# Kernel tuning notes

Hardware: AMD Instinct MI355X
Metric: run time of the kernel (lower is better)

The kernel has to match this reference:

```python
import jax, jax.numpy as jnp
from jax import lax
import numpy as np

B, H, W = 2048, 28, 28
LATENT_EACH = 64
LATENT = 2 * LATENT_EACH  # 128
MEM_SIZE = 8192
TOPK = 10
EPS = 1e-12


def _conv(x, w, b):
    # x: NCHW, w: OIHW, 3x3 conv, padding=1 (SAME)
    y = lax.conv_general_dilated(x, w, (1, 1), 'SAME',
                                 dimension_numbers=('NCHW', 'OIHW', 'NCHW'))
    return y + b[None, :, None, None]


def _deconv(x, w, b):
    # ConvTranspose2d(k=4, stride=2, padding=1) -> out = 2*in (SAME transpose)
    # w: HWIO = (4,4,in,out)
    y = lax.conv_transpose(x, w, (2, 2), 'SAME',
                           dimension_numbers=('NCHW', 'HWIO', 'NCHW'))
    return y + b[None, :, None, None]


def _encoder(x, w1, b1, w2, b2, fcw, fcb):
    h = jax.nn.relu(_conv(x, w1, b1))
    h = jax.nn.relu(_conv(h, w2, b2))
    feat = h.mean(axis=(2, 3))  # AdaptiveAvgPool2d((1,1)) + flatten -> [B,64]
    return feat @ fcw.T + fcb


def _memory_match(z, mem):
    mn = mem / jnp.maximum(jnp.linalg.norm(mem, axis=1, keepdims=True), EPS)
    zn = z / jnp.maximum(jnp.linalg.norm(z, axis=1, keepdims=True), EPS)
    sim = zn @ mn.T                      # [B, MEM_SIZE]
    topv, topi = lax.top_k(sim, TOPK)    # [B, K]
    wts = jax.nn.softmax(topv, axis=1)   # [B, K]
    sel = mem[topi]                      # gather: [B, K, LATENT]
    return jnp.einsum('bk,bkd->bd', wts, sel)


def setup_inputs() -> dict:
    key = jax.random.key(0)
    ks = jax.random.split(key, 24)
    g = lambda k, s, scale=0.05: jax.random.normal(k, s, jnp.float32) * scale
    inp = {
        'x': jax.random.normal(ks[0], (B, 1, H, W), jnp.float32),
        # center encoder
        'ce_w1': g(ks[1], (32, 1, 3, 3)), 'ce_b1': jnp.zeros((32,), jnp.float32),
        'ce_w2': g(ks[2], (64, 32, 3, 3)), 'ce_b2': jnp.zeros((64,), jnp.float32),
        'ce_fcw': g(ks[3], (LATENT_EACH, 64)), 'ce_fcb': jnp.zeros((LATENT_EACH,), jnp.float32),
        # global encoder
        'ge_w1': g(ks[4], (32, 1, 3, 3)), 'ge_b1': jnp.zeros((32,), jnp.float32),
        'ge_w2': g(ks[5], (64, 32, 3, 3)), 'ge_b2': jnp.zeros((64,), jnp.float32),
        'ge_fcw': g(ks[6], (LATENT_EACH, 64)), 'ge_fcb': jnp.zeros((LATENT_EACH,), jnp.float32),
        # memory bank (Parameter ~ randn)
        'mem': jax.random.normal(ks[7], (MEM_SIZE, LATENT), jnp.float32),
        # decoder
        'dec_fcw': g(ks[8], (64 * 7 * 7, LATENT)), 'dec_fcb': jnp.zeros((64 * 7 * 7,), jnp.float32),
        'd_w1': g(ks[9], (4, 4, 64, 32)), 'd_b1': jnp.zeros((32,), jnp.float32),   # deconv 64->32
        'd_w2': g(ks[10], (16, 32, 3, 3)), 'd_b2': jnp.zeros((16,), jnp.float32),  # conv 32->16
        'd_w3': g(ks[11], (4, 4, 16, 8)), 'd_b3': jnp.zeros((8,), jnp.float32),    # deconv 16->8
        'd_w4': g(ks[12], (1, 8, 3, 3)), 'd_b4': jnp.zeros((1,), jnp.float32),     # conv 8->1
    }
    return inp


def reference(x, ce_w1, ce_b1, ce_w2, ce_b2, ce_fcw, ce_fcb,
              ge_w1, ge_b1, ge_w2, ge_b2, ge_fcw, ge_fcb,
              mem, dec_fcw, dec_fcb,
              d_w1, d_b1, d_w2, d_b2, d_w3, d_b3, d_w4, d_b4):
    # crop_center(x, 14): start = (28-14)//2 = 7
    x_center = x[:, :, 7:21, 7:21]
    z_center = _encoder(x_center, ce_w1, ce_b1, ce_w2, ce_b2, ce_fcw, ce_fcb)
    z_global = _encoder(x, ge_w1, ge_b1, ge_w2, ge_b2, ge_fcw, ge_fcb)
    z = jnp.concatenate([z_center, z_global], axis=1)  # [B, 128]
    z_match = _memory_match(z, mem)                    # [B, 128]
    d = (z_match @ dec_fcw.T + dec_fcb).reshape(B, 64, 7, 7)
    d = jax.nn.relu(_deconv(d, d_w1, d_b1))   # [B,32,14,14]
    d = jax.nn.relu(_conv(d, d_w2, d_b2))     # [B,16,14,14]
    d = jax.nn.relu(_deconv(d, d_w3, d_b3))   # [B,8,28,28]
    x_hat = _conv(d, d_w4, d_b4)              # [B,1,28,28]
    return x_hat
```

## Files before the change

kernel.cpp:

```cpp
#include <hip/hip_runtime.h>
#include <cfloat>
#include <cmath>

#define TPB 256

typedef _Float16 half8 __attribute__((ext_vector_type(8)));
typedef float floatx16 __attribute__((ext_vector_type(16)));
typedef float floatx4 __attribute__((ext_vector_type(4)));

__device__ __forceinline__ float wave_reduce_sum(float v) {
#pragma unroll
  for (int off = 32; off > 0; off >>= 1) v += __shfl_xor(v, off, 64);
  return v;
}

__global__ __launch_bounds__(64) void prep_bfrags(
    const float* __restrict__ ce_w2, const float* __restrict__ ge_w2,
    float* __restrict__ frags) {
  const int blk = blockIdx.x;
  const int enc = blk / 72;
  const int frag = blk % 72;
  const int ks = frag >> 2, part = (frag >> 1) & 1, nt = frag & 1;
  const int tap = ks >> 1, half = ks & 1;
  const int lane = threadIdx.x;
  const float* w2 = enc ? ge_w2 : ce_w2;
  const int n = nt * 32 + (lane & 31);
  const int cb = half * 16 + (lane >> 5) * 8;
  half8 out;
#pragma unroll
  for (int j = 0; j < 8; ++j) {
    float v = w2[(n * 32 + cb + j) * 9 + tap];
    _Float16 h = (_Float16)v;
    out[j] = (part == 0) ? h : (_Float16)((v - (float)h) * 4096.f);
  }
  *(half8*)((char*)frags + ((size_t)blk * 64 + lane) * 16) = out;
}

__global__ __launch_bounds__(64) void prep_dec1(
    const float* __restrict__ w1, float* __restrict__ frags) {
  const int blk = blockIdx.x;
  const int phase = blk >> 4, ks = blk & 15;
  const int pa = phase >> 1, pb = phase & 1;
  const int st = ks >> 2, kk = ks & 3;
  const int s = st >> 1, tt = st & 1;
  const int lane = threadIdx.x;
  const int kg = lane >> 5, n = lane & 31;
  const int tap = (pa + 2 * s) * 4 + (pb + 2 * tt);
  half8 o;
#pragma unroll
  for (int j = 0; j < 8; ++j) {
    int c = kk * 16 + kg * 8 + j;
    o[j] = (_Float16)w1[tap * 2048 + c * 32 + n];
  }
  *(half8*)((char*)frags + ((size_t)blk * 64 + lane) * 16) = o;
}

__global__ __launch_bounds__(64) void prep_dfc(
    const float* __restrict__ dfcw, float* __restrict__ frags) {
  const int blk = blockIdx.x;
  const int nt = blk >> 3, ks = blk & 7;
  const int lane = threadIdx.x;
  const int n = lane & 31, kg = lane >> 5;
  const int j = nt * 32 + n;
  const int px = j >> 6, c = j & 63;
  half8 o;
#pragma unroll
  for (int u = 0; u < 8; ++u)
    o[u] = (_Float16)dfcw[(size_t)(c * 49 + px) * 128 + ks * 16 + kg * 8 + u];
  *(half8*)((char*)frags + ((size_t)blk * 64 + lane) * 16) = o;
}

__global__ __launch_bounds__(64) void prep_mem(
    const float* __restrict__ memg, float* __restrict__ frags) {
  const int blk = blockIdx.x;
  const int slot = blk & 15;
  const int p = slot >> 3, ks = slot & 7;
  const int T = blk >> 4;
  const int lane = threadIdx.x;
  const int n = lane & 31, kg = lane >> 5;
  const float* src = memg + (size_t)(T * 32 + n) * 128 + ks * 16 + kg * 8;
  half8 o;
#pragma unroll
  for (int j = 0; j < 8; ++j) {
    float v = src[j];
    _Float16 h = (_Float16)v;
    o[j] = p ? (_Float16)((v - (float)h) * 4096.f) : h;
  }
  *(half8*)((char*)frags + ((size_t)blk * 64 + lane) * 16) = o;
}

__global__ __launch_bounds__(256) void norm_kernel(
    const float* __restrict__ memg, float* __restrict__ invn) {
  const int wv = threadIdx.x >> 6, lane = threadIdx.x & 63;
  const int row = blockIdx.x * 4 + wv;
  const float* r = memg + (size_t)row * 128;
  float a = r[lane], b = r[lane + 64];
  float s = wave_reduce_sum(a * a + b * b);
  if (lane == 0) invn[row] = 1.f / fmaxf(sqrtf(s), 1e-12f);
}

template <int S, bool CENTER>
__device__ __forceinline__ void encoder_body(
    char* smem, const float* __restrict__ x, const float* __restrict__ w1,
    const float* __restrict__ b1, const float* __restrict__ b2,
    const float* __restrict__ fcw, const float* __restrict__ fcb,
    const float* __restrict__ bfrag, float* __restrict__ zout, int zoff,
    int b) {
  constexpr int SP = S + 2;
  constexpr int NBANDS = (S == 28) ? 3 : 2;
  constexpr int RMAX = 12;
  constexpr int NPIX = RMAX * SP;
  constexpr int GSTB = NPIX * 16;
  constexpr int PSTB = 4 * GSTB;

  char* h1s = smem;
  float* xs = (float*)(smem + 2 * PSTB);
  float* w1s = xs + SP * SP;
  float* featp = w1s + 288;

  const int t = threadIdx.x;
  const int lane = t & 63;
  const int wv = t >> 6;
  const int ntW = wv & 1;

  for (int e = t; e < SP * SP; e += TPB) xs[e] = 0.f;
  for (int e = t; e < 288; e += TPB) w1s[e] = w1[e];
  __syncthreads();
  const float* xb = x + (size_t)b * 784 + (CENTER ? (7 * 28 + 7) : 0);
  for (int e = t; e < S * S; e += TPB) {
    int i = e / S, j = e - i * S;
    xs[(i + 1) * SP + (j + 1)] = xb[i * 28 + j];
  }

  float sp = 0.f;
  const float biasW = b2[ntW * 32 + (lane & 31)];
  const int gOff = (lane >> 5) * GSTB;
  const char* bgbase = (const char*)bfrag + lane * 16;

#pragma unroll
  for (int band = 0; band < NBANDS; ++band) {
    const int BH_ = (S == 28) ? ((band < 2) ? 10 : 8) : ((band == 0) ? 10 : 4);
    const int b0 = band * 10;
    const int LIMIT = BH_ * S;
    const int MTB = (LIMIT + 31) / 32;

    __syncthreads();
    for (int e = t; e < 4 * NPIX; e += TPB) {
      int g = e / NPIX;
      int pix = e - g * NPIX;
      int lr = pix / SP;
      int cw = pix - lr * SP;
      int gr = b0 - 1 + lr;
      int ebase = g * GSTB + pix * 16;
      half8 hi8 = {}, lo8 = {};
      if (gr >= 0 && gr < S && cw >= 1 && cw <= S) {
        float xv[9];
#pragma unroll
        for (int di = 0; di < 3; ++di)
#pragma unroll
          for (int dj = 0; dj < 3; ++dj)
            xv[di * 3 + dj] = xs[(gr + di) * SP + (cw - 1 + dj)];
#pragma unroll
        for (int u = 0; u < 8; ++u) {
          int ch = g * 8 + u;
          float a = b1[ch];
#pragma unroll
          for (int v = 0; v < 9; ++v) a += xv[v] * w1s[ch * 9 + v];
          a = fmaxf(a, 0.f);
          _Float16 h = (_Float16)a;
          hi8[u] = h;
          lo8[u] = (_Float16)((a - (float)h) * 4096.f);
        }
      }
      *(half8*)(h1s + ebase) = hi8;
      *(half8*)(h1s + PSTB + ebase) = lo8;
    }
    __syncthreads();
#pragma unroll 1
    for (int u = wv; u < 2 * MTB; u += 4) {
      const int mt = u >> 1;
      floatx16 accH = {}, accL = {};
      int px = mt * 32 + (lane & 31);
      px = px < LIMIT ? px : LIMIT - 1;
      const int r = px / S, cc = px - r * S;
      const int pixB = (r * SP + cc) * 16;
#pragma unroll 3
      for (int tap = 0; tap < 9; ++tap) {
        const int di = tap / 3, dj = tap - di * 3;
        const int offT = (di * SP + dj) * 16;
#pragma unroll
        for (int half = 0; half < 2; ++half) {
          const int ks = tap * 2 + half;
          const char* bp = bgbase + ks * 4096 + ntW * 1024;
          const int offA = pixB + offT + gOff + half * (2 * GSTB);
          half8 ah = *(const half8*)(h1s + offA);
          half8 al = *(const half8*)(h1s + PSTB + offA);
          half8 bh = *(const half8*)(bp);
          half8 bl = *(const half8*)(bp + 2048);
          accH = __builtin_amdgcn_mfma_f32_32x32x16_f16(ah, bh, accH, 0, 0, 0);
          accL = __builtin_amdgcn_mfma_f32_32x32x16_f16(ah, bl, accL, 0, 0, 0);
          accL = __builtin_amdgcn_mfma_f32_32x32x16_f16(al, bh, accL, 0, 0, 0);
        }
      }
#pragma unroll
      for (int reg = 0; reg < 16; ++reg) {
        int row = (reg & 3) + 8 * (reg >> 2) + 4 * (lane >> 5);
        int p = mt * 32 + row;
        if (p < LIMIT)
          sp += fmaxf(accH[reg] + accL[reg] * (1.f / 4096.f) + biasW, 0.f);
      }
    }
  }
  sp += __shfl_xor(sp, 32);
  if (lane < 32) featp[wv * 32 + lane] = sp;
  __syncthreads();
  if (t < 64) featp[t] = (featp[t] + featp[64 + t]) * (1.f / (S * S));
  __syncthreads();
  if (t < 64) {
    float s = 0.f;
#pragma unroll
    for (int i = 0; i < 64; ++i) s += featp[i] * fcw[t * 64 + i];
    zout[(size_t)b * 128 + zoff + t] = s + fcb[t];
  }
}

__global__ __launch_bounds__(256, 3) void encoders_fused(
    const float* __restrict__ x, const float* __restrict__ ce_w1,
    const float* __restrict__ ce_b1, const float* __restrict__ ce_b2,
    const float* __restrict__ ce_fcw, const float* __restrict__ ce_fcb,
    const float* __restrict__ ge_w1, const float* __restrict__ ge_b1,
    const float* __restrict__ ge_b2, const float* __restrict__ ge_fcw,
    const float* __restrict__ ge_fcb, const float* __restrict__ frags,
    float* __restrict__ z) {
  __shared__ __align__(16) char smem[51344];
  if (blockIdx.x < 2048)
    encoder_body<28, false>(smem, x, ge_w1, ge_b1, ge_b2, ge_fcw, ge_fcb,
                            frags + 18432, z, 64, blockIdx.x);
  else
    encoder_body<14, true>(smem, x, ce_w1, ce_b1, ce_b2, ce_fcw, ce_fcb, frags,
                           z, 0, blockIdx.x - 2048);
}

__global__ __launch_bounds__(256) void match_mfma(
    const float* __restrict__ z, const float* __restrict__ memfrags,
    const float* __restrict__ invn, float* __restrict__ topvw,
    int* __restrict__ topiw) {
  __shared__ __align__(16) char smem[49408];
  float* zs = (float*)smem;
  float* qv = (float*)smem;
  int* qi = (int*)(smem + 16384);
  char* zfrag = smem + 32768;
  float* rowmin = (float*)(smem + 49152);
  int* qn = (int*)(smem + 49152 + 128);

  const int t = threadIdx.x;
  const int lane = t & 63;
  const int wv = t >> 6;
  const int rowbase = blockIdx.x * 32;
  const int Tbase = blockIdx.y * 16;

  for (int e = t; e < 4096; e += TPB) zs[e] = z[(size_t)rowbase * 128 + e];
  if (t < 32) { rowmin[t] = -FLT_MAX; qn[t] = 0; }
  __syncthreads();
#pragma unroll
  for (int h = 0; h < 8; ++h) {
    int r = wv * 8 + h;
    float a = zs[r * 128 + lane], b = zs[r * 128 + 64 + lane];
    float s = wave_reduce_sum(a * a + b * b);
    float inv = 1.f / fmaxf(sqrtf(s), 1e-12f);
    zs[r * 128 + lane] = a * inv;
    zs[r * 128 + 64 + lane] = b * inv;
  }
  __syncthreads();
  for (int e = t; e < 4096; e += TPB) {
    int m = e >> 7, c = e & 127;
    float v = zs[m * 128 + c];
    _Float16 h = (_Float16)v;
    _Float16 l = (_Float16)((v - (float)h) * 4096.f);
    int ks = c >> 4, kg = (c >> 3) & 1, j = c & 7;
    int off = (ks * 64 + kg * 32 + m) * 16 + j * 2;
    *(_Float16*)(zfrag + off) = h;
    *(_Float16*)(zfrag + 8192 + off) = l;
  }
  __syncthreads();

  half8 ah[8], al[8];
  {
    const char* zf = zfrag + ((lane >> 5) * 32 + (lane & 31)) * 16;
#pragma unroll
    for (int ks = 0; ks < 8; ++ks) {
      ah[ks] = *(const half8*)(zf + ks * 1024);
      al[ks] = *(const half8*)(zf + 8192 + ks * 1024);
    }
  }

  float av[10];
  int ai[10];
#pragma unroll
  for (int i = 0; i < 10; ++i) { av[i] = -FLT_MAX; ai[i] = 0; }

#pragma unroll 1
  for (int round = 0; round < 4; ++round) {
    const int T = Tbase + round * 4 + wv;
    const char* bf = (const char*)memfrags + (size_t)T * 16384 + lane * 16;
    floatx16 acc0 = {}, acc1 = {};
#pragma unroll
    for (int ks = 0; ks < 8; ++ks) {
      half8 bh = *(const half8*)(bf + ks * 1024);
      half8 bl = *(const half8*)(bf + 8192 + ks * 1024);
      acc0 = __builtin_amdgcn_mfma_f32_32x32x16_f16(ah[ks], bh, acc0, 0, 0, 0);
      acc1 = __builtin_amdgcn_mfma_f32_32x32x16_f16(ah[ks], bl, acc1, 0, 0, 0);
      acc1 = __builtin_amdgcn_mfma_f32_32x32x16_f16(al[ks], bh, acc1, 0, 0, 0);
    }
    const int gn = T * 32 + (lane & 31);
    const float iv = invn[gn];
#pragma unroll
    for (int reg = 0; reg < 16; ++reg) {
      int m = (reg & 3) + 8 * (reg >> 2) + 4 * (lane >> 5);
      float v = (acc0[reg] + acc1[reg] * (1.f / 4096.f)) * iv;
      if (v > rowmin[m]) {
        int k = atomicAdd(&qn[m], 1);
        qv[m * 128 + k] = v;
        qi[m * 128 + k] = gn;
      }
    }
    __syncthreads();
    if (t < 32) {
      int n = qn[t];
      for (int k = 0; k < n; ++k) {
        float v = qv[t * 128 + k];
        int mm = qi[t * 128 + k];
        if (v > av[9]) {
#pragma unroll
          for (int i = 0; i < 10; ++i) {
            if (v > av[i]) {
              float tv = av[i]; av[i] = v; v = tv;
              int ti = ai[i]; ai[i] = mm; mm = ti;
            }
          }
        }
      }
      qn[t] = 0;
      rowmin[t] = av[9];
    }
    __syncthreads();
  }

  if (t < 32) {
    const size_t base = (size_t)(rowbase + t) * 160 + blockIdx.y * 10;
#pragma unroll
    for (int k = 0; k < 10; ++k) {
      topvw[base + k] = av[k];
      topiw[base + k] = ai[k];
    }
  }
}

__global__ __launch_bounds__(256) void match_merge(
    const float* __restrict__ topvw, const int* __restrict__ topiw,
    const float* __restrict__ memg, _Float16* __restrict__ zmf16) {
  __shared__ float topw[8][10];
  __shared__ int topidx[8][10];
  const int t = threadIdx.x;
  const int rowbase = blockIdx.x * 8;

  if (t < 8) {
    float av[10];
    int ai[10];
#pragma unroll
    for (int i = 0; i < 10; ++i) { av[i] = -FLT_MAX; ai[i] = 0; }
    const size_t base = (size_t)(rowbase + t) * 160;
    for (int c = 0; c < 160; ++c) {
      float v = topvw[base + c];
      int m = topiw[base + c];
      if (v > av[9]) {
#pragma unroll
        for (int i = 0; i < 10; ++i) {
          if (v > av[i]) {
            float tv = av[i]; av[i] = v; v = tv;
            int ti = ai[i]; ai[i] = m; m = ti;
          }
        }
      }
    }
    float e_[10], s = 0.f;
#pragma unroll
    for (int k = 0; k < 10; ++k) { e_[k] = expf(av[k]); s += e_[k]; }
    float inv = 1.f / s;
#pragma unroll
    for (int k = 0; k < 10; ++k) { topw[t][k] = e_[k] * inv; topidx[t][k] = ai[k]; }
  }
  __syncthreads();
  for (int e = t; e < 8 * 128; e += TPB) {
    int r = e >> 7, d = e & 127;
    float o = 0.f;
#pragma unroll
    for (int k = 0; k < 10; ++k)
      o += topw[r][k] * memg[(size_t)topidx[r][k] * 128 + d];
    zmf16[(size_t)(rowbase + r) * 128 + d] = (_Float16)o;
  }
}

__global__ __launch_bounds__(256) void decfc_kernel(
    const _Float16* __restrict__ zmf16, const float* __restrict__ fcb,
    const float* __restrict__ dfcfrags, _Float16* __restrict__ d0f16) {
  const int t = threadIdx.x;
  const int lane = t & 63;
  const int wv = t >> 6;
  const int r0 = blockIdx.x * 32;
  const int ntbase = blockIdx.y * 49;

  half8 a[8];
  {
    const _Float16* ap =
        zmf16 + (size_t)(r0 + (lane & 31)) * 128 + (lane >> 5) * 8;
#pragma unroll
    for (int ks = 0; ks < 8; ++ks) a[ks] = *(const half8*)(ap + ks * 16);
  }
  const char* fb = (const char*)dfcfrags + lane * 16;

  for (int nt = ntbase + wv; nt < ntbase + 49; nt += 4) {
    half8 bfr[8];
    const char* p = fb + (size_t)nt * 8192;
#pragma unroll
    for (int ks = 0; ks < 8; ++ks) bfr[ks] = *(const half8*)(p + ks * 1024);
    floatx16 acc = {};
#pragma unroll
    for (int ks = 0; ks < 8; ++ks)
      acc = __builtin_amdgcn_mfma_f32_32x32x16_f16(a[ks], bfr[ks], acc, 0, 0, 0);
    const int col = nt * 32 + (lane & 31);
    const int px = col >> 6, c = col & 63;
    const float bias = fcb[c * 49 + px];
#pragma unroll
    for (int reg = 0; reg < 16; ++reg) {
      int row = (reg & 3) + 8 * (reg >> 2) + 4 * (lane >> 5);
      d0f16[((size_t)(r0 + row) * 49 + px) * 64 + c] = (_Float16)(acc[reg] + bias);
    }
  }
}

__global__ __launch_bounds__(256) void decoder_kernel(
    const _Float16* __restrict__ d0f16, const float* __restrict__ b1,
    const float* __restrict__ w2, const float* __restrict__ b2,
    const float* __restrict__ w3, const float* __restrict__ b3,
    const float* __restrict__ w4, const float* __restrict__ b4,
    const float* __restrict__ dec1frags, float* __restrict__ out) {
  __shared__ __align__(16) char dsm[41408];
  char* d0f = dsm;
  float* d2 = (float*)dsm;
  char* d1f = dsm + 12608;
  char* w2s = dsm + 28992;
  float* d3 = (float*)(dsm + 12608);

  const int b = blockIdx.x;
  const int t = threadIdx.x;
  const int lane = t & 63;
  const int wv = t >> 6;

  for (int e = t; e < 648; e += TPB) {
    int g = e / 81, pix = e - g * 81;
    int ih = pix / 9 - 1, iw = pix % 9 - 1;
    half8 hv = {};
    if (ih >= 0 && ih < 7 && iw >= 0 && iw < 7)
      hv = *(const half8*)(d0f16 + ((size_t)b * 49 + ih * 7 + iw) * 64 + g * 8);
    *(half8*)(d0f + e * 16) = hv;
  }
  for (int e = t; e < 576; e += TPB) {
    int tau = e / 64, l = e - tau * 64;
    int n = l & 15, kq = l >> 4;
    half8 v;
#pragma unroll
    for (int u = 0; u < 8; ++u)
      v[u] = (_Float16)w2[(n * 32 + kq * 8 + u) * 9 + tau];
    *(half8*)(w2s + e * 16) = v;
  }
  for (int e = t; e < 1024; e += TPB)
    *(float4*)(d1f + e * 16) = make_float4(0.f, 0.f, 0.f, 0.f);
  __syncthreads();

  {
    const int pa = wv >> 1, pb = wv & 1;
    const int kg = lane >> 5, o = lane & 31;
    const char* bg = (const char*)dec1frags + wv * 16384 + lane * 16;
    int pxa[2][4];
#pragma unroll
    for (int im = 0; im < 2; ++im) {
      int px = im * 32 + o;
      px = px < 49 ? px : 48;
      int i = px / 7, j2 = px - i * 7;
#pragma unroll
      for (int st = 0; st < 4; ++st) {
        int s = st >> 1, tt = st & 1;
        pxa[im][st] = ((i + pa + s) * 9 + (j2 + pb + tt)) * 16;
      }
    }
    floatx16 acc0 = {}, acc1 = {};
    half8 nb = *(const half8*)(bg);
#pragma unroll
    for (int ks = 0; ks < 16; ++ks) {
      half8 bf = nb;
      if (ks < 15) nb = *(const half8*)(bg + (ks + 1) * 1024);
      const int gbase = (((ks & 3) * 2 + kg) * 81) * 16;
      half8 a0 = *(const half8*)(d0f + gbase + pxa[0][ks >> 2]);
      half8 a1 = *(const half8*)(d0f + gbase + pxa[1][ks >> 2]);
      acc0 = __builtin_amdgcn_mfma_f32_32x32x16_f16(a0, bf, acc0, 0, 0, 0);
      acc1 = __builtin_amdgcn_mfma_f32_32x32x16_f16(a1, bf, acc1, 0, 0, 0);
    }
    const float bias = b1[o];
    char* dst = d1f + (o >> 3) * 4096 + (o & 7) * 2;
#pragma unroll
    for (int im = 0; im < 2; ++im) {
      const floatx16& ac = im ? acc1 : acc0;
#pragma unroll
      for (int reg = 0; reg < 16; ++reg) {
        int row = (reg & 3) + 8 * (reg >> 2) + 4 * kg;
        int px = im * 32 + row;
        if (px < 49) {
          int i = px / 7, j2 = px - i * 7;
          int p = 2 * i + pa, q = 2 * j2 + pb;
          *(_Float16*)(dst + ((p + 1) * 16 + (q + 1)) * 16) =
              (_Float16)fmaxf(ac[reg] + bias, 0.f);
        }
      }
    }
  }
  __syncthreads();

  {
    const int m = lane & 15, kq = lane >> 4;
    half8 bq[9];
#pragma unroll
    for (int tau = 0; tau < 9; ++tau)
      bq[tau] = *(const half8*)(w2s + (tau * 64 + lane) * 16);
    for (int mt = wv; mt < 13; mt += 4) {
      int px = mt * 16 + m;
      px = px < 196 ? px : 195;
      const int p = px / 14, q = px - (px / 14) * 14;
      floatx4 acc = {};
#pragma unroll
      for (int tau = 0; tau < 9; ++tau) {
        const int dp = tau / 3, dq = tau - dp * 3;
        half8 av =
            *(const half8*)(d1f + (kq * 256 + (p + dp) * 16 + (q + dq)) * 16);
        acc = __builtin_amdgcn_mfma_f32_16x16x32_f16(av, bq[tau], acc, 0, 0, 0);
      }
      const int o = lane & 15;
      const float bias = b2[o];
#pragma unroll
      for (int reg = 0; reg < 4; ++reg) {
        int row = (lane >> 4) * 4 + reg;
        int opx = mt * 16 + row;
        if (opx < 196) d2[o * 197 + opx] = fmaxf(acc[reg] + bias, 0.f);
      }
    }
  }
  __syncthreads();
  for (int e = t; e < 7200; e += TPB) d3[e] = 0.f;
  __syncthreads();

  {
    const int ph = __builtin_amdgcn_readfirstlane(t >> 6);
    const int pa = ph >> 1, pb = ph & 1;
    const int tb = pa * 4 + pb;
    const float* wA = w3 + (size_t)tb * 128;
    const float* wB = w3 + (size_t)(tb + 2) * 128;
    const float* wC = w3 + (size_t)(tb + 8) * 128;
    const float* wD = w3 + (size_t)(tb + 10) * 128;
#pragma unroll 1
    for (int k = 0; k < 4; ++k) {
      const int px = lane + 64 * k;
      const int cpx = px < 196 ? px : 195;
      const int i = cpx / 14, j = cpx % 14;
      int ih[2], iw[2];
      float mh[2], mw[2];
#pragma unroll
      for (int s = 0; s < 2; ++s) {
        int v = i + pa + s - 1;
        mh[s] = (v >= 0 && v <= 13) ? 1.f : 0.f;
        ih[s] = v < 0 ? 0 : (v > 13 ? 13 : v);
        int u = j + pb + s - 1;
        mw[s] = (u >= 0 && u <= 13) ? 1.f : 0.f;
        iw[s] = u < 0 ? 0 : (u > 13 ? 13 : u);
      }
      const float m00 = mh[0] * mw[0], m01 = mh[0] * mw[1];
      const float m10 = mh[1] * mw[0], m11 = mh[1] * mw[1];
      float acc[8];
#pragma unroll
      for (int oo = 0; oo < 8; ++oo) acc[oo] = b3[oo];
#pragma unroll 2
      for (int c = 0; c < 16; ++c) {
        const float a00 = d2[c * 197 + ih[0] * 14 + iw[0]] * m00;
        const float a01 = d2[c * 197 + ih[0] * 14 + iw[1]] * m01;
        const float a10 = d2[c * 197 + ih[1] * 14 + iw[0]] * m10;
        const float a11 = d2[c * 197 + ih[1] * 14 + iw[1]] * m11;
        const int wb = c * 8;
#pragma unroll
        for (int oo = 0; oo < 8; ++oo)
          acc[oo] += a00 * wA[wb + oo] + a01 * wB[wb + oo] +
                     a10 * wC[wb + oo] + a11 * wD[wb + oo];
      }
      if (px < 196) {
        const int p = 2 * i + pa, q = 2 * j + pb;
        const int widx = (p + 1) * 30 + (q + 1);
#pragma unroll
        for (int oo = 0; oo < 8; ++oo)
          d3[oo * 900 + widx] = fmaxf(acc[oo], 0.f);
      }
    }
  }
  __syncthreads();

  for (int e = t; e < 784; e += TPB) {
    int p = e / 28, q = e - p * 28;
    float a = b4[0];
#pragma unroll
    for (int c = 0; c < 8; ++c) {
      const float* bp = &d3[c * 900 + p * 30 + q];
#pragma unroll
      for (int di = 0; di < 3; ++di)
#pragma unroll
        for (int dj = 0; dj < 3; ++dj)
          a += bp[di * 30 + dj] * w4[c * 9 + di * 3 + dj];
    }
    out[(size_t)b * 784 + e] = a;
  }
}

extern "C" void kernel_launch(void* const* d_in, const int* in_sizes, int n_in,
                              void* d_out, int out_size, void* d_ws,
                              size_t ws_size, hipStream_t stream) {
  const float* x      = (const float*)d_in[0];
  const float* ce_w1  = (const float*)d_in[1];
  const float* ce_b1  = (const float*)d_in[2];
  const float* ce_w2  = (const float*)d_in[3];
  const float* ce_b2  = (const float*)d_in[4];
  const float* ce_fcw = (const float*)d_in[5];
  const float* ce_fcb = (const float*)d_in[6];
  const float* ge_w1  = (const float*)d_in[7];
  const float* ge_b1  = (const float*)d_in[8];
  const float* ge_w2  = (const float*)d_in[9];
  const float* ge_b2  = (const float*)d_in[10];
  const float* ge_fcw = (const float*)d_in[11];
  const float* ge_fcb = (const float*)d_in[12];
  const float* memg   = (const float*)d_in[13];
  const float* dfcw   = (const float*)d_in[14];
  const float* dfcb   = (const float*)d_in[15];
  const float* d_w1   = (const float*)d_in[16];
  const float* d_b1   = (const float*)d_in[17];
  const float* d_w2   = (const float*)d_in[18];
  const float* d_b2   = (const float*)d_in[19];
  const float* d_w3   = (const float*)d_in[20];
  const float* d_b3   = (const float*)d_in[21];
  const float* d_w4   = (const float*)d_in[22];
  const float* d_b4   = (const float*)d_in[23];
  float* outp = (float*)d_out;

  float*     ws        = (float*)d_ws;
  float*     z         = ws;
  _Float16*  zmf16     = (_Float16*)(ws + 262144);
  float*     invn      = ws + 262144 + 131072;
  float*     frags     = invn + 8192;
  float*     dec1frags = frags + 36864;
  float*     dfcfrags  = dec1frags + 16384;
  float*     memfrags  = dfcfrags + 200704;
  float*     tailbase  = memfrags + 1048576;
  float*     topvw     = tailbase;
  int*       topiw     = (int*)(tailbase + 327680);
  _Float16*  d0f16     = (_Float16*)tailbase;

  prep_bfrags<<<144, 64, 0, stream>>>(ce_w2, ge_w2, frags);
  prep_dec1<<<64, 64, 0, stream>>>(d_w1, dec1frags);
  prep_dfc<<<784, 64, 0, stream>>>(dfcw, dfcfrags);
  prep_mem<<<4096, 64, 0, stream>>>(memg, memfrags);
  norm_kernel<<<2048, TPB, 0, stream>>>(memg, invn);
  encoders_fused<<<4096, TPB, 0, stream>>>(x, ce_w1, ce_b1, ce_b2, ce_fcw,
                                           ce_fcb, ge_w1, ge_b1, ge_b2, ge_fcw,
                                           ge_fcb, frags, z);
  match_mfma<<<dim3(64, 16), TPB, 0, stream>>>(z, memfrags, invn, topvw, topiw);
  match_merge<<<256, TPB, 0, stream>>>(topvw, topiw, memg, zmf16);
  decfc_kernel<<<dim3(64, 2), TPB, 0, stream>>>(zmf16, dfcb, dfcfrags, d0f16);
  decoder_kernel<<<2048, TPB, 0, stream>>>(d0f16, d_b1, d_w2, d_b2, d_w3, d_b3,
                                           d_w4, d_b4, dec1frags, outp);
}
```

Before: 661.3 us.

## Use uniform 7-row bands and compute both output-channel tiles per wave

The encoder conv2 now processes the image in uniform 7-row bands (4 for the global encoder, 2 for the center), which shrinks the fp16 split-precision staging buffer in shared memory. Each wave now computes both 32-channel output tiles for its pixel tile, reusing the A fragments across two sets of MFMAs instead of splitting channels across waves. The smaller LDS footprint allows raising the occupancy hint from 3 to 4 blocks per CU. The cost is more accumulator registers per wave (four floatx16), which may cause register pressure or spills under the tighter launch bound, and a final reduction over four partial feature rows.

```diff
diff --git a/kernel.cpp b/kernel.cpp
--- a/kernel.cpp
+++ b/kernel.cpp
@@ -107,11 +107,12 @@
     const float* __restrict__ bfrag, float* __restrict__ zout, int zoff,
     int b) {
   constexpr int SP = S + 2;
-  constexpr int NBANDS = (S == 28) ? 3 : 2;
-  constexpr int RMAX = 12;
-  constexpr int NPIX = RMAX * SP;
+  constexpr int NBANDS = S / 7;
+  constexpr int NPIX = 9 * SP;
   constexpr int GSTB = NPIX * 16;
   constexpr int PSTB = 4 * GSTB;
+  constexpr int LIMIT = 7 * S;
+  constexpr int MTB = (LIMIT + 31) / 32;
 
   char* h1s = smem;
   float* xs = (float*)(smem + 2 * PSTB);
@@ -121,7 +122,6 @@
   const int t = threadIdx.x;
   const int lane = t & 63;
   const int wv = t >> 6;
-  const int ntW = wv & 1;
 
   for (int e = t; e < SP * SP; e += TPB) xs[e] = 0.f;
   for (int e = t; e < 288; e += TPB) w1s[e] = w1[e];
@@ -132,17 +132,15 @@
     xs[(i + 1) * SP + (j + 1)] = xb[i * 28 + j];
   }
 
-  float sp = 0.f;
-  const float biasW = b2[ntW * 32 + (lane & 31)];
+  float sp0 = 0.f, sp1 = 0.f;
+  const float bias0 = b2[lane & 31];
+  const float bias1 = b2[32 + (lane & 31)];
   const int gOff = (lane >> 5) * GSTB;
   const char* bgbase = (const char*)bfrag + lane * 16;
 
-#pragma unroll
+#pragma unroll 1
   for (int band = 0; band < NBANDS; ++band) {
-    const int BH_ = (S == 28) ? ((band < 2) ? 10 : 8) : ((band == 0) ? 10 : 4);
-    const int b0 = band * 10;
-    const int LIMIT = BH_ * S;
-    const int MTB = (LIMIT + 31) / 32;
+    const int b0 = band * 7;
 
     __syncthreads();
     for (int e = t; e < 4 * NPIX; e += TPB) {
@@ -177,9 +175,8 @@
     }
     __syncthreads();
 #pragma unroll 1
-    for (int u = wv; u < 2 * MTB; u += 4) {
-      const int mt = u >> 1;
-      floatx16 accH = {}, accL = {};
+    for (int mt = wv; mt < MTB; mt += 4) {
+      floatx16 aH0 = {}, aL0 = {}, aH1 = {}, aL1 = {};
       int px = mt * 32 + (lane & 31);
       px = px < LIMIT ? px : LIMIT - 1;
       const int r = px / S, cc = px - r * S;
@@ -191,30 +188,47 @@
 #pragma unroll
         for (int half = 0; half < 2; ++half) {
           const int ks = tap * 2 + half;
-          const char* bp = bgbase + ks * 4096 + ntW * 1024;
+          const char* bp = bgbase + ks * 4096;
           const int offA = pixB + offT + gOff + half * (2 * GSTB);
           half8 ah = *(const half8*)(h1s + offA);
           half8 al = *(const half8*)(h1s + PSTB + offA);
-          half8 bh = *(const half8*)(bp);
-          half8 bl = *(const half8*)(bp + 2048);
-          accH = __builtin_amdgcn_mfma_f32_32x32x16_f16(ah, bh, accH, 0, 0, 0);
-          accL = __builtin_amdgcn_mfma_f32_32x32x16_f16(ah, bl, accL, 0, 0, 0);
-          accL = __builtin_amdgcn_mfma_f32_32x32x16_f16(al, bh, accL, 0, 0, 0);
+          {
+            half8 bh = *(const half8*)(bp);
+            half8 bl = *(const half8*)(bp + 2048);
+            aH0 = __builtin_amdgcn_mfma_f32_32x32x16_f16(ah, bh, aH0, 0, 0, 0);
+            aL0 = __builtin_amdgcn_mfma_f32_32x32x16_f16(ah, bl, aL0, 0, 0, 0);
+            aL0 = __builtin_amdgcn_mfma_f32_32x32x16_f16(al, bh, aL0, 0, 0, 0);
+          }
+          {
+            half8 bh = *(const half8*)(bp + 1024);
+            half8 bl = *(const half8*)(bp + 3072);
+            aH1 = __builtin_amdgcn_mfma_f32_32x32x16_f16(ah, bh, aH1, 0, 0, 0);
+            aL1 = __builtin_amdgcn_mfma_f32_32x32x16_f16(ah, bl, aL1, 0, 0, 0);
+            aL1 = __builtin_amdgcn_mfma_f32_32x32x16_f16(al, bh, aL1, 0, 0, 0);
+          }
         }
       }
 #pragma unroll
       for (int reg = 0; reg < 16; ++reg) {
         int row = (reg & 3) + 8 * (reg >> 2) + 4 * (lane >> 5);
         int p = mt * 32 + row;
-        if (p < LIMIT)
-          sp += fmaxf(accH[reg] + accL[reg] * (1.f / 4096.f) + biasW, 0.f);
-      }
-    }
-  }
-  sp += __shfl_xor(sp, 32);
-  if (lane < 32) featp[wv * 32 + lane] = sp;
-  __syncthreads();
-  if (t < 64) featp[t] = (featp[t] + featp[64 + t]) * (1.f / (S * S));
+        if (p < LIMIT) {
+          sp0 += fmaxf(aH0[reg] + aL0[reg] * (1.f / 4096.f) + bias0, 0.f);
+          sp1 += fmaxf(aH1[reg] + aL1[reg] * (1.f / 4096.f) + bias1, 0.f);
+        }
+      }
+    }
+  }
+  sp0 += __shfl_xor(sp0, 32);
+  sp1 += __shfl_xor(sp1, 32);
+  if (lane < 32) {
+    featp[wv * 64 + lane] = sp0;
+    featp[wv * 64 + 32 + lane] = sp1;
+  }
+  __syncthreads();
+  if (t < 64)
+    featp[t] = (featp[t] + featp[64 + t] + featp[128 + t] + featp[192 + t]) *
+               (1.f / (S * S));
   __syncthreads();
   if (t < 64) {
     float s = 0.f;
@@ -224,7 +238,7 @@
   }
 }
 
-__global__ __launch_bounds__(256, 3) void encoders_fused(
+__global__ __launch_bounds__(256, 4) void encoders_fused(
     const float* __restrict__ x, const float* __restrict__ ce_w1,
     const float* __restrict__ ce_b1, const float* __restrict__ ce_b2,
     const float* __restrict__ ce_fcw, const float* __restrict__ ce_fcb,
@@ -232,7 +246,7 @@
     const float* __restrict__ ge_b2, const float* __restrict__ ge_fcw,
     const float* __restrict__ ge_fcb, const float* __restrict__ frags,
     float* __restrict__ z) {
-  __shared__ __align__(16) char smem[51344];
+  __shared__ __align__(16) char smem[40336];
   if (blockIdx.x < 2048)
     encoder_body<28, false>(smem, x, ge_w1, ge_b1, ge_b2, ge_fcw, ge_fcb,
                             frags + 18432, z, 64, blockIdx.x);
```

New measurement: 669.7 us. Within noise of the previous version (+1.3%).
